# Optimization experiments

Measured on AMD Instinct MI355X. Metric: run time of the kernel, lower is better.

## Reference

```python
import jax, jax.numpy as jnp
import numpy as np

H = 512      # hidden == embed (required: process-block LSTM consumes attention output of size hidden)
XY = 2
CITY_T = 100
BATCH = 512
INIT = 0.08  # uniform(-0.08, 0.08) weight init


def _unif(key, shape):
    return jax.random.uniform(key, shape, jnp.float32, minval=-INIT, maxval=INIT)


def lstm_cell(x, h, c, Wih, Whh, bih, bhh):
    # PyTorch gate order: i, f, g, o
    g = x @ Wih.T + h @ Whh.T + (bih + bhh)
    i, f, gg, o = jnp.split(g, 4, axis=-1)
    c_new = jax.nn.sigmoid(f) * c + jax.nn.sigmoid(i) * jnp.tanh(gg)
    h_new = jax.nn.sigmoid(o) * jnp.tanh(c_new)
    return h_new, c_new


def setup_inputs() -> dict:
    key = jax.random.key(0)
    ks = jax.random.split(key, 20)
    inp = {
        "x": jax.random.uniform(ks[0], (BATCH, CITY_T, XY), jnp.float32),      # city coords in [0,1)
        "dec_i1": jax.random.uniform(ks[1], (BATCH, H), jnp.float32),          # torch.rand(batch,1,hidden)
        "W_emb": _unif(ks[2], (H, XY)),
        "enc_Wih": _unif(ks[3], (4 * H, H)),
        "enc_Whh": _unif(ks[4], (4 * H, H)),
        "enc_bih": _unif(ks[5], (4 * H,)),
        "enc_bhh": _unif(ks[6], (4 * H,)),
        "dec_Wih": _unif(ks[7], (4 * H, H)),
        "dec_Whh": _unif(ks[8], (4 * H, H)),
        "dec_bih": _unif(ks[9], (4 * H,)),
        "dec_bhh": _unif(ks[10], (4 * H,)),
        "W_q": _unif(ks[11], (H, H)),
        "W_ref": _unif(ks[12], (H, H)),
        "v": _unif(ks[13], (1, H)),       # Vec: Linear(hidden,1,bias=False)
        "fc1": _unif(ks[14], (H, H)),
        "fc2": _unif(ks[15], (1, H)),
    }
    return inp


def reference(x, dec_i1, W_emb, enc_Wih, enc_Whh, enc_bih, enc_bhh,
              dec_Wih, dec_Whh, dec_bih, dec_bhh, W_q, W_ref, v, fc1, fc2):
    batch, city_t, _ = x.shape
    emb = x @ W_emb.T                                   # (b, c, H)

    # ---- Encoder LSTM (zero initial state) ----
    h0 = jnp.zeros((batch, H), emb.dtype)
    c0 = jnp.zeros((batch, H), emb.dtype)

    def enc_step(carry, xt):
        h, c = carry
        h, c = lstm_cell(xt, h, c, enc_Wih, enc_Whh, enc_bih, enc_bhh)
        return (h, c), h

    (hT, cT), enc_h = jax.lax.scan(enc_step, (h0, c0), jnp.swapaxes(emb, 0, 1))
    enc_h = jnp.swapaxes(enc_h, 0, 1)                   # (b, c, H)

    # W_ref(enc_h) is static across decode steps -> compute once
    u1 = enc_h @ W_ref.T                                # (b, c, H)

    # ---- Decoder: city_t steps of LSTM cell + Bahdanau attention ----
    def dec_step(carry, _):
        dec_i, h, c = carry
        h, c = lstm_cell(dec_i, h, c, dec_Wih, dec_Whh, dec_bih, dec_bhh)
        u2 = h @ W_q.T                                  # (b, H)
        u = jnp.tanh(u1 + u2[:, None, :]) @ v[0]        # (b, c)
        a = jax.nn.softmax(u, axis=1)
        d = jnp.einsum('bc,bch->bh', a, enc_h)          # glimpse (b, H)
        return (d, h, c), None

    (_, h_last, _), _ = jax.lax.scan(dec_step, (dec_i1, hT, cT), None, length=city_t)

    # final2FC: Linear->ReLU->Linear -> scalar per batch
    pred_l = jax.nn.relu(h_last @ fc1.T) @ fc2.T        # (b, 1)
    return pred_l[:, 0]
```

## Files before the change

kernel.cpp:

```cpp
#include <hip/hip_runtime.h>
#include <hip/hip_bf16.h>

#define H 512
#define TSTEPS 100
#define BATCH 512
#define KB 16
#define NBLK 256
#define NT 512
#define NGRP 8
#define GBLK 32

typedef __attribute__((ext_vector_type(8))) short bf16x8;
typedef __attribute__((ext_vector_type(8))) unsigned short u16x8;
typedef __attribute__((ext_vector_type(4))) float f32x4;
typedef unsigned short u16;

__device__ __forceinline__ float bf2f(u16 u) {
    union { unsigned int i; float f; } z; z.i = ((unsigned int)u) << 16; return z.f;
}
__device__ __forceinline__ u16 f2bf(float f) {
    union { float f; unsigned int u; } z; z.f = f;
    unsigned int r = (z.u + 0x7fffu + ((z.u >> 16) & 1u)) >> 16;
    return (u16)r;
}
__device__ __forceinline__ float sigmoidf_(float x) { return 1.0f / (1.0f + __expf(-x)); }
__device__ __forceinline__ float ftanh(float x) {
    x = fminf(15.0f, fmaxf(-15.0f, x));
    float e = __expf(2.0f * x);
    return (e - 1.0f) / (e + 1.0f);
}
__device__ __forceinline__ f32x4 MF(bf16x8 a, bf16x8 b, f32x4 c) {
    return __builtin_amdgcn_mfma_f32_16x16x32_bf16(a, b, c, 0, 0, 0);
}

__device__ __forceinline__ size_t pidx(int m, int k) {
    int kb = k >> 5, kin = k & 31;
    int lane = (m & 15) + (((kin >> 2) & 3) << 4);
    int j = (kin & 3) + ((kin >> 4) << 2);
    return ((size_t)((m >> 4) * KB + kb) * 64 + lane) * 8 + j;
}

__device__ __forceinline__ void gbar32(unsigned* bar, int grp) {
    __syncthreads();
    if (threadIdx.x == 0) {
        unsigned* cnt = &bar[grp * 32];
        unsigned* gen = &bar[grp * 32 + 16];
        unsigned g = __hip_atomic_load(gen, __ATOMIC_RELAXED, __HIP_MEMORY_SCOPE_AGENT);
        if (__hip_atomic_fetch_add(cnt, 1u, __ATOMIC_ACQ_REL, __HIP_MEMORY_SCOPE_AGENT) == GBLK - 1u) {
            __hip_atomic_store(cnt, 0u, __ATOMIC_RELAXED, __HIP_MEMORY_SCOPE_AGENT);
            __hip_atomic_fetch_add(gen, 1u, __ATOMIC_ACQ_REL, __HIP_MEMORY_SCOPE_AGENT);
        } else {
            while (__hip_atomic_load(gen, __ATOMIC_RELAXED, __HIP_MEMORY_SCOPE_AGENT) == g) {
                __builtin_amdgcn_s_sleep(2);
            }
            __threadfence();
        }
    }
    __syncthreads();
}

__global__ void prep_kernel(const float* __restrict__ W_emb, const float* __restrict__ enc_Wih,
                            const float* __restrict__ enc_bih, const float* __restrict__ enc_bhh,
                            const float* __restrict__ dec_bih, const float* __restrict__ dec_bhh,
                            float* __restrict__ Wc, float* __restrict__ bc, float* __restrict__ db) {
    int g = blockIdx.x * blockDim.x + threadIdx.x;
    if (g >= 4 * H) return;
    float s0 = 0.f, s1 = 0.f;
    for (int j = 0; j < H; ++j) {
        float w = enc_Wih[(size_t)g * H + j];
        s0 += w * W_emb[j * 2 + 0];
        s1 += w * W_emb[j * 2 + 1];
    }
    Wc[g * 2 + 0] = s0; Wc[g * 2 + 1] = s1;
    bc[g] = enc_bih[g] + enc_bhh[g];
    db[g] = dec_bih[g] + dec_bhh[g];
}

__global__ void pack_w(const float* __restrict__ W, u16* __restrict__ hi, u16* __restrict__ lo,
                       int total) {
    int idx = blockIdx.x * 256 + threadIdx.x;
    if (idx >= total) return;
    int m = idx >> 9, k = idx & 511;
    float v = W[idx];
    u16 h16 = f2bf(v);
    u16 l16 = f2bf(v - bf2f(h16));
    size_t p = pidx(m, k);
    hi[p] = h16; lo[p] = l16;
}

__global__ void zero4(float* __restrict__ p, int n) {
    int i = blockIdx.x * blockDim.x + threadIdx.x;
    if (i < n) p[i] = 0.f;
}

__global__ __launch_bounds__(NT, 1) void persist_enc(
    const float* __restrict__ x, const float* __restrict__ Wc, const float* __restrict__ bc,
    const u16* __restrict__ WeH, const u16* __restrict__ WeL,
    float* __restrict__ cbuf, u16* __restrict__ hbuf,
    u16* __restrict__ ench, unsigned* __restrict__ bar) {
    extern __shared__ char smem[];
    u16* wlds = (u16*)smem;
    float* exch = (float*)(smem + 131072);
    const int tid = threadIdx.x;
    const int lane = tid & 63;
    const int w = tid >> 6;
    const int q = w & 3, jh = w >> 2;
    const int blk = blockIdx.x;
    const int grp = blk & 7, nni = blk >> 3;
    const size_t BHs = (size_t)BATCH * H;

    for (int c = 0; c < 8; ++c) {
        int cq = c >> 1, hl = c & 1;
        const u16x8* s8 = (const u16x8*)((hl ? WeL : WeH) + (size_t)((cq * 32 + nni) * KB) * 512);
        u16x8* d8 = (u16x8*)(wlds + c * 8192);
        for (int i = tid; i < 1024; i += NT) d8[i] = s8[i];
    }
    __syncthreads();

    for (int t = 0; t < TSTEPS; ++t) {
        const u16* Ah = hbuf + (size_t)(t & 1) * 2 * BHs;
        const u16* Al = Ah + BHs;
        u16* Hh = hbuf + (size_t)((t + 1) & 1) * 2 * BHs;
        u16* Hl = Hh + BHs;
        f32x4 acc[2] = {};
#pragma unroll 4
        for (int kb = 0; kb < KB; ++kb) {
            bf16x8 bh = *(const bf16x8*)&wlds[((q * 2 + 0) * KB + kb) * 512 + lane * 8];
            bf16x8 bl = *(const bf16x8*)&wlds[((q * 2 + 1) * KB + kb) * 512 + lane * 8];
#pragma unroll
            for (int jj = 0; jj < 2; ++jj) {
                int j = jh * 2 + jj;
                size_t ab = ((size_t)((grp * 4 + j) * KB + kb) * 64 + lane) * 8;
                bf16x8 ah = *(const bf16x8*)&Ah[ab];
                bf16x8 al = *(const bf16x8*)&Al[ab];
                acc[jj] = MF(ah, bh, acc[jj]);
                acc[jj] = MF(ah, bl, acc[jj]);
                acc[jj] = MF(al, bh, acc[jj]);
            }
        }
        const int col = lane & 15, rg = lane >> 4;
#pragma unroll
        for (int jj = 0; jj < 2; ++jj)
#pragma unroll
            for (int r = 0; r < 4; ++r)
                exch[(q * 64 + (jh * 2 + jj) * 16 + rg * 4 + r) * 16 + col] = acc[jj][r];
        __syncthreads();
#pragma unroll
        for (int k = 0; k < 2; ++k) {
            int cell = k * NT + tid;
            int lb = cell >> 4, cl = cell & 15;
            int b = grp * 64 + lb, n = nni * 16 + cl;
            float x0 = x[((size_t)b * TSTEPS + t) * 2 + 0];
            float x1 = x[((size_t)b * TSTEPS + t) * 2 + 1];
            float g[4];
#pragma unroll
            for (int qq = 0; qq < 4; ++qq)
                g[qq] = exch[(qq * 64 + lb) * 16 + cl] + bc[qq * H + n]
                      + x0 * Wc[(qq * H + n) * 2 + 0] + x1 * Wc[(qq * H + n) * 2 + 1];
            size_t ci = (size_t)b * H + n;
            float cn = sigmoidf_(g[1]) * cbuf[ci] + sigmoidf_(g[0]) * ftanh(g[2]);
            float hn = sigmoidf_(g[3]) * ftanh(cn);
            cbuf[ci] = cn;
            u16 hh = f2bf(hn), hl16 = f2bf(hn - bf2f(hh));
            size_t p = pidx(b, n);
            Hh[p] = hh; Hl[p] = hl16;
            ench[((size_t)b * TSTEPS + t) * H + n] = hh;
        }
        gbar32(bar, grp);
    }
}

__global__ __launch_bounds__(NT, 1) void persist_dec(
    const u16* __restrict__ WdiH, const u16* __restrict__ WdiL,
    const u16* __restrict__ WdhH, const u16* __restrict__ WdhL,
    const float* __restrict__ db,
    const u16* __restrict__ WqH, const u16* __restrict__ WqL,
    const u16* __restrict__ u1r, const u16* __restrict__ ench, const float* __restrict__ vv,
    float* __restrict__ cbuf, u16* __restrict__ hbuf,
    u16* __restrict__ dhi, u16* __restrict__ dlo,
    unsigned* __restrict__ bar) {
    extern __shared__ char smem[];
    u16* wlds = (u16*)smem;
    char* scratch = smem + 131072;
    float* exch  = (float*)scratch;
    float* u2row = (float*)scratch;
    float* ssc   = (float*)(scratch + 4096);
    float* ssm   = (float*)(scratch + 4928);
    f32x4* dacc  = (f32x4*)(scratch + 5760);
    const int tid = threadIdx.x;
    const int lane = tid & 63;
    const int w = tid >> 6;
    const int blk = blockIdx.x;
    const int grp = blk & 7, nni = blk >> 3;
    const size_t BHs = (size_t)BATCH * H;

    float vvr[8];
    {
        float4 v0 = *(const float4*)&vv[lane * 8];
        float4 v1 = *(const float4*)&vv[lane * 8 + 4];
        vvr[0] = v0.x; vvr[1] = v0.y; vvr[2] = v0.z; vvr[3] = v0.w;
        vvr[4] = v1.x; vvr[5] = v1.y; vvr[6] = v1.z; vvr[7] = v1.w;
    }

    for (int c = 0; c < 8; ++c) {
        int mat = c >> 2, cq = c & 3;
        const u16x8* s8 = (const u16x8*)((mat ? WdhH : WdiH) + (size_t)((cq * 32 + nni) * KB) * 512);
        u16x8* d8 = (u16x8*)(wlds + c * 8192);
        for (int i = tid; i < 1024; i += NT) d8[i] = s8[i];
    }
    __syncthreads();

    for (int s = 0; s < TSTEPS; ++s) {
        {
            const u16* hAh = hbuf + (size_t)(s & 1) * 2 * BHs;
            const u16* hAl = hAh + BHs;
            u16* Hh = hbuf + (size_t)((s + 1) & 1) * 2 * BHs;
            u16* Hl = Hh + BHs;
            const int q = w & 3, jh = w >> 2;
            f32x4 acc[2] = {};
#pragma unroll
            for (int ph = 0; ph < 2; ++ph) {
                const u16* Ah = ph ? hAh : dhi;
                const u16* Al = ph ? hAl : dlo;
                const u16* Wl = ph ? WdhL : WdiL;
#pragma unroll 4
                for (int kb = 0; kb < KB; ++kb) {
                    bf16x8 bh = *(const bf16x8*)&wlds[((ph * 4 + q) * KB + kb) * 512 + lane * 8];
                    bf16x8 bl = *(const bf16x8*)&Wl[((size_t)((q * 32 + nni) * KB + kb) * 64 + lane) * 8];
#pragma unroll
                    for (int jj = 0; jj < 2; ++jj) {
                        int j = jh * 2 + jj;
                        size_t ab = ((size_t)((grp * 4 + j) * KB + kb) * 64 + lane) * 8;
                        bf16x8 ah = *(const bf16x8*)&Ah[ab];
                        bf16x8 al = *(const bf16x8*)&Al[ab];
                        acc[jj] = MF(ah, bh, acc[jj]);
                        acc[jj] = MF(ah, bl, acc[jj]);
                        acc[jj] = MF(al, bh, acc[jj]);
                    }
                }
            }
            const int col = lane & 15, rg = lane >> 4;
#pragma unroll
            for (int jj = 0; jj < 2; ++jj)
#pragma unroll
                for (int r = 0; r < 4; ++r)
                    exch[(q * 64 + (jh * 2 + jj) * 16 + rg * 4 + r) * 16 + col] = acc[jj][r];
            __syncthreads();
#pragma unroll
            for (int k = 0; k < 2; ++k) {
                int cell = k * NT + tid;
                int lb = cell >> 4, cl = cell & 15;
                int b = grp * 64 + lb, n = nni * 16 + cl;
                float g[4];
#pragma unroll
                for (int qq = 0; qq < 4; ++qq)
                    g[qq] = exch[(qq * 64 + lb) * 16 + cl] + db[qq * H + n];
                size_t ci = (size_t)b * H + n;
                float cn = sigmoidf_(g[1]) * cbuf[ci] + sigmoidf_(g[0]) * ftanh(g[2]);
                float hn = sigmoidf_(g[3]) * ftanh(cn);
                cbuf[ci] = cn;
                u16 hh = f2bf(hn), hl16 = f2bf(hn - bf2f(hh));
                size_t p = pidx(b, n);
                Hh[p] = hh; Hl[p] = hl16;
            }
        }
        if (s == TSTEPS - 1) break;
        gbar32(bar, grp);

        {
            const u16* Ah = hbuf + (size_t)((s + 1) & 1) * 2 * BHs;
            const u16* Al = Ah + BHs;
            const int mf = grp * 4 + (nni >> 3);
            f32x4 acc[4] = {};
#pragma unroll 4
            for (int kb = 0; kb < KB; ++kb) {
                size_t ab = ((size_t)(mf * KB + kb) * 64 + lane) * 8;
                bf16x8 ah = *(const bf16x8*)&Ah[ab];
                bf16x8 al = *(const bf16x8*)&Al[ab];
#pragma unroll
                for (int f = 0; f < 4; ++f) {
                    int n16 = w * 4 + f;
                    size_t fb = ((size_t)(n16 * KB + kb) * 64 + lane) * 8;
                    bf16x8 bh = *(const bf16x8*)&WqH[fb];
                    bf16x8 bl = *(const bf16x8*)&WqL[fb];
                    acc[f] = MF(ah, bh, acc[f]);
                    acc[f] = MF(ah, bl, acc[f]);
                    acc[f] = MF(al, bh, acc[f]);
                }
            }
            const int col = lane & 15, rg = lane >> 4;
            const int t0 = (nni & 7) * 2;
#pragma unroll
            for (int f = 0; f < 4; ++f)
#pragma unroll
                for (int r = 0; r < 4; ++r) {
                    int m = rg * 4 + r;
                    int n = (w * 4 + f) * 16 + col;
                    if (m == t0)     u2row[n] = acc[f][r];
                    if (m == t0 + 1) u2row[512 + n] = acc[f][r];
                }
        }
        __syncthreads();
        {
            const int r = tid >> 8;
            const int par = (tid >> 6) & 3;
            const int ccb = par * 25;
            const int b = grp * 64 + 2 * nni + r;
            float u2v[8];
            {
                float4 a0 = *(const float4*)&u2row[r * 512 + lane * 8];
                float4 a1 = *(const float4*)&u2row[r * 512 + lane * 8 + 4];
                u2v[0] = a0.x; u2v[1] = a0.y; u2v[2] = a0.z; u2v[3] = a0.w;
                u2v[4] = a1.x; u2v[5] = a1.y; u2v[6] = a1.z; u2v[7] = a1.w;
            }
            const u16* u1base = &u1r[(size_t)b * TSTEPS * H + lane * 8];
            const u16* ehbase = &ench[(size_t)b * TSTEPS * H + lane * 8];
            for (int i0 = 0; i0 < 25; i0 += 5) {
                u16x8 uvv[5];
#pragma unroll
                for (int u = 0; u < 5; ++u)
                    uvv[u] = *(const u16x8*)&u1base[(size_t)(ccb + i0 + u) * H];
#pragma unroll
                for (int u = 0; u < 5; ++u) {
                    float pp = 0.f;
#pragma unroll
                    for (int j = 0; j < 8; ++j)
                        pp += vvr[j] * ftanh(bf2f(uvv[u][j]) + u2v[j]);
#pragma unroll
                    for (int off = 32; off; off >>= 1) pp += __shfl_xor(pp, off);
                    if (lane == 0) ssc[r * 100 + ccb + i0 + u] = pp;
                }
            }
            __syncthreads();
            if (tid < 128) {
                int r2 = tid >> 6, ln = tid & 63;
                float s1 = ssc[r2 * 100 + ln];
                float s2 = (ln + 64 < 100) ? ssc[r2 * 100 + ln + 64] : -1e30f;
                float m = fmaxf(s1, s2);
#pragma unroll
                for (int off = 32; off; off >>= 1) m = fmaxf(m, __shfl_xor(m, off));
                float e1 = __expf(s1 - m);
                float e2 = (ln + 64 < 100) ? __expf(s2 - m) : 0.f;
                float sum = e1 + e2;
#pragma unroll
                for (int off = 32; off; off >>= 1) sum += __shfl_xor(sum, off);
                float inv = 1.f / sum;
                ssm[r2 * 100 + ln] = e1 * inv;
                if (ln + 64 < 100) ssm[r2 * 100 + ln + 64] = e2 * inv;
            }
            __syncthreads();
            float ga[8] = {};
            for (int i0 = 0; i0 < 25; i0 += 5) {
                u16x8 evv[5];
#pragma unroll
                for (int u = 0; u < 5; ++u)
                    evv[u] = *(const u16x8*)&ehbase[(size_t)(ccb + i0 + u) * H];
#pragma unroll
                for (int u = 0; u < 5; ++u) {
                    float a = ssm[r * 100 + ccb + i0 + u];
#pragma unroll
                    for (int j = 0; j < 8; ++j) ga[j] += a * bf2f(evv[u][j]);
                }
            }
            f32x4 g0 = {ga[0], ga[1], ga[2], ga[3]};
            f32x4 g1 = {ga[4], ga[5], ga[6], ga[7]};
            dacc[(((par * 2 + r) * 64) + lane) * 2 + 0] = g0;
            dacc[(((par * 2 + r) * 64) + lane) * 2 + 1] = g1;
            __syncthreads();
            if (tid < 128) {
                int r2 = tid >> 6, l = tid & 63;
                float fin[8];
#pragma unroll
                for (int j = 0; j < 8; ++j) fin[j] = 0.f;
#pragma unroll
                for (int pq = 0; pq < 4; ++pq) {
                    f32x4 d0 = dacc[(((pq * 2 + r2) * 64) + l) * 2 + 0];
                    f32x4 d1 = dacc[(((pq * 2 + r2) * 64) + l) * 2 + 1];
                    fin[0] += d0[0]; fin[1] += d0[1]; fin[2] += d0[2]; fin[3] += d0[3];
                    fin[4] += d1[0]; fin[5] += d1[1]; fin[6] += d1[2]; fin[7] += d1[3];
                }
                int b2 = grp * 64 + 2 * nni + r2;
                int h0 = l * 8;
#pragma unroll
                for (int qd = 0; qd < 2; ++qd) {
                    int k = h0 + 4 * qd;
                    size_t p = (((size_t)(b2 >> 4) * KB + (k >> 5)) * 64 + (b2 & 15)
                                + (((k >> 2) & 3) << 4)) * 8 + (((k >> 4) & 1) << 2);
                    float f0 = fin[4 * qd], f1 = fin[4 * qd + 1], f2 = fin[4 * qd + 2], f3 = fin[4 * qd + 3];
                    u16 a0 = f2bf(f0), a1 = f2bf(f1), a2 = f2bf(f2), a3 = f2bf(f3);
                    *(ushort4*)&dhi[p] = make_ushort4(a0, a1, a2, a3);
                    u16 c0 = f2bf(f0 - bf2f(a0)), c1 = f2bf(f1 - bf2f(a1));
                    u16 c2 = f2bf(f2 - bf2f(a2)), c3 = f2bf(f3 - bf2f(a3));
                    *(ushort4*)&dlo[p] = make_ushort4(c0, c1, c2, c3);
                }
            }
        }
        gbar32(bar, grp);
    }
}

__global__ __launch_bounds__(256) void gemm_u1(const u16* __restrict__ ench_row,
                                               const u16* __restrict__ Bh, const u16* __restrict__ Bl,
                                               u16* __restrict__ u1_row) {
    __shared__ u16 lds[2 * KB * 64 * 8];
    const int tid = threadIdx.x;
    const int m0 = blockIdx.x * 32;
    {
        int r = tid >> 3;
        int o = tid & 7;
#pragma unroll
        for (int p8 = 0; p8 < 8; ++p8) {
            int k0 = (o + 8 * p8) * 8;
            const u16* src = &ench_row[(size_t)(m0 + r) * H + k0];
            ushort4 v0 = *(const ushort4*)&src[0];
            ushort4 v1 = *(const ushort4*)&src[4];
            int kb = k0 >> 5, kin0 = k0 & 31;
            int g0 = (kin0 >> 2) & 3;
            int jo = (kin0 >> 4) << 2;
            u16* base = &lds[(size_t)(((r >> 4) * KB + kb) * 64) * 8];
            *(ushort4*)&base[((r & 15) + 16 * g0) * 8 + jo] = v0;
            *(ushort4*)&base[((r & 15) + 16 * (g0 + 1)) * 8 + jo] = v1;
        }
    }
    __syncthreads();
    const int lane = tid & 63;
    const int w = tid >> 6;
    const int mw = w & 1, nh = w >> 1;
    for (int nc = 0; nc < 16; ++nc) {
        int n16 = nh * 16 + nc;
        f32x4 acc = {};
#pragma unroll 4
        for (int kb = 0; kb < KB; ++kb) {
            bf16x8 a = *(const bf16x8*)&lds[((mw * KB + kb) * 64 + lane) * 8];
            size_t fb = ((size_t)(n16 * KB + kb) * 64 + lane) * 8;
            bf16x8 bh = *(const bf16x8*)&Bh[fb];
            bf16x8 bl = *(const bf16x8*)&Bl[fb];
            acc = MF(a, bh, acc);
            acc = MF(a, bl, acc);
        }
        const int col = lane & 15, rg = lane >> 4;
#pragma unroll
        for (int r = 0; r < 4; ++r) {
            size_t mrow = (size_t)m0 + mw * 16 + rg * 4 + r;
            u1_row[mrow * H + n16 * 16 + col] = f2bf(acc[r]);
        }
    }
}

__global__ __launch_bounds__(256) void final_kernel(const u16* __restrict__ hi,
                                                    const u16* __restrict__ lo,
                                                    const float* __restrict__ fc1,
                                                    const float* __restrict__ fc2,
                                                    float* __restrict__ out) {
    const int b = blockIdx.x;
    __shared__ float hsh[H];
    __shared__ float red[256];
    for (int i = threadIdx.x; i < H; i += 256) {
        size_t p = pidx(b, i);
        hsh[i] = bf2f(hi[p]) + bf2f(lo[p]);
    }
    __syncthreads();
    float total = 0.f;
    for (int n = threadIdx.x; n < H; n += 256) {
        float acc = 0.f;
        for (int j = 0; j < H; ++j) acc += fc1[(size_t)n * H + j] * hsh[j];
        total += fmaxf(acc, 0.f) * fc2[n];
    }
    red[threadIdx.x] = total;
    __syncthreads();
    for (int s = 128; s > 0; s >>= 1) {
        if (threadIdx.x < s) red[threadIdx.x] += red[threadIdx.x + s];
        __syncthreads();
    }
    if (threadIdx.x == 0) out[b] = red[0];
}

extern "C" void kernel_launch(void* const* d_in, const int* in_sizes, int n_in,
                              void* d_out, int out_size, void* d_ws, size_t ws_size,
                              hipStream_t stream) {
    (void)in_sizes; (void)n_in; (void)out_size;
    const float* x       = (const float*)d_in[0];
    const float* dec_i1  = (const float*)d_in[1];
    const float* W_emb   = (const float*)d_in[2];
    const float* enc_Wih = (const float*)d_in[3];
    const float* enc_Whh = (const float*)d_in[4];
    const float* enc_bih = (const float*)d_in[5];
    const float* enc_bhh = (const float*)d_in[6];
    const float* dec_Wih = (const float*)d_in[7];
    const float* dec_Whh = (const float*)d_in[8];
    const float* dec_bih = (const float*)d_in[9];
    const float* dec_bhh = (const float*)d_in[10];
    const float* W_q     = (const float*)d_in[11];
    const float* W_ref   = (const float*)d_in[12];
    const float* vv      = (const float*)d_in[13];
    const float* fc1     = (const float*)d_in[14];
    const float* fc2     = (const float*)d_in[15];
    float* out = (float*)d_out;

    const size_t BH = (size_t)BATCH * H;
    const size_t W4 = (size_t)4 * H * H;
    const size_t WS = (size_t)H * H;
    const size_t TBH = (size_t)TSTEPS * BATCH * H;

    unsigned* bar = (unsigned*)d_ws;
    float* c_  = (float*)d_ws + 256;
    u16* hbuf  = (u16*)(c_ + BH);
    float* Wc  = (float*)(hbuf + 4 * BH);
    float* bc  = Wc + 4 * H * 2;
    float* db  = bc + 4 * H;
    u16* dhi   = (u16*)(db + 4 * H);
    u16* dlo   = dhi + BH;
    u16* WeH   = dlo + BH;    u16* WeL  = WeH + W4;
    u16* WdiH  = WeL + W4;    u16* WdiL = WdiH + W4;
    u16* WdhH  = WdiL + W4;   u16* WdhL = WdhH + W4;
    u16* WqH   = WdhL + W4;   u16* WqL  = WqH + WS;
    u16* WrH   = WqL + WS;    u16* WrL  = WrH + WS;
    u16* ench  = WrL + WS;
    u16* u1r   = ench + TBH;

    size_t needed = (size_t)((char*)(u1r + TBH) - (char*)d_ws);
    if (ws_size < needed) return;

    const int ENC_SMEM = 131072 + 16384;
    const int DEC_SMEM = 131072 + 22528;
    (void)hipFuncSetAttribute((const void*)persist_enc, hipFuncAttributeMaxDynamicSharedMemorySize, ENC_SMEM);
    (void)hipFuncSetAttribute((const void*)persist_dec, hipFuncAttributeMaxDynamicSharedMemorySize, DEC_SMEM);

    prep_kernel<<<8, 256, 0, stream>>>(W_emb, enc_Wih, enc_bih, enc_bhh, dec_bih, dec_bhh, Wc, bc, db);
    pack_w<<<(int)(W4 / 256), 256, 0, stream>>>(enc_Whh, WeH, WeL, (int)W4);
    pack_w<<<(int)(W4 / 256), 256, 0, stream>>>(dec_Wih, WdiH, WdiL, (int)W4);
    pack_w<<<(int)(W4 / 256), 256, 0, stream>>>(dec_Whh, WdhH, WdhL, (int)W4);
    pack_w<<<(int)(WS / 256), 256, 0, stream>>>(W_q, WqH, WqL, (int)WS);
    pack_w<<<(int)(WS / 256), 256, 0, stream>>>(W_ref, WrH, WrL, (int)WS);
    pack_w<<<(int)(BH / 256), 256, 0, stream>>>(dec_i1, dhi, dlo, (int)BH);
    zero4<<<(int)((256 + 3 * BH + 255) / 256), 256, 0, stream>>>((float*)d_ws, (int)(256 + 3 * BH));

    persist_enc<<<NBLK, NT, ENC_SMEM, stream>>>(x, Wc, bc, WeH, WeL, c_, hbuf, ench, bar);
    gemm_u1<<<TSTEPS * BATCH / 32, 256, 0, stream>>>(ench, WrH, WrL, u1r);
    persist_dec<<<NBLK, NT, DEC_SMEM, stream>>>(WdiH, WdiL, WdhH, WdhL, db, WqH, WqL,
                                                u1r, ench, vv, c_, hbuf, dhi, dlo, bar);
    final_kernel<<<BATCH, 256, 0, stream>>>(hbuf, hbuf + BH, fc1, fc2, out);
}
```

Measured before the change: 13.19 ms.

## Double block size to 1024 threads and redistribute per-wave work

Raises threads per block from 512 to 1024 in the persistent encoder and decoder kernels. Each wave now computes one MFMA tile instead of two, the gate and cell update runs one cell per thread, the W_q projection uses two output tiles per wave instead of four, and the attention score and glimpse loops spread cities across 8 partitions in an interleaved order instead of 4 contiguous ones. The aim is more waves in flight per CU to hide memory latency in the serial recurrent steps. In exchange it adds an extra LDS reduction pass with an additional __syncthreads, and it may raise register pressure at 1024 threads per block.

```diff
diff --git a/kernel.cpp b/kernel.cpp
--- a/kernel.cpp
+++ b/kernel.cpp
@@ -6,7 +6,7 @@
 #define BATCH 512
 #define KB 16
 #define NBLK 256
-#define NT 512
+#define NT 1024
 #define NGRP 8
 #define GBLK 32
 
@@ -104,7 +104,7 @@
     const int tid = threadIdx.x;
     const int lane = tid & 63;
     const int w = tid >> 6;
-    const int q = w & 3, jh = w >> 2;
+    const int q = w & 3, j = w >> 2;
     const int blk = blockIdx.x;
     const int grp = blk & 7, nni = blk >> 3;
     const size_t BHs = (size_t)BATCH * H;
@@ -122,33 +122,25 @@
         const u16* Al = Ah + BHs;
         u16* Hh = hbuf + (size_t)((t + 1) & 1) * 2 * BHs;
         u16* Hl = Hh + BHs;
-        f32x4 acc[2] = {};
+        f32x4 acc = {};
 #pragma unroll 4
         for (int kb = 0; kb < KB; ++kb) {
             bf16x8 bh = *(const bf16x8*)&wlds[((q * 2 + 0) * KB + kb) * 512 + lane * 8];
             bf16x8 bl = *(const bf16x8*)&wlds[((q * 2 + 1) * KB + kb) * 512 + lane * 8];
-#pragma unroll
-            for (int jj = 0; jj < 2; ++jj) {
-                int j = jh * 2 + jj;
-                size_t ab = ((size_t)((grp * 4 + j) * KB + kb) * 64 + lane) * 8;
-                bf16x8 ah = *(const bf16x8*)&Ah[ab];
-                bf16x8 al = *(const bf16x8*)&Al[ab];
-                acc[jj] = MF(ah, bh, acc[jj]);
-                acc[jj] = MF(ah, bl, acc[jj]);
-                acc[jj] = MF(al, bh, acc[jj]);
-            }
+            size_t ab = ((size_t)((grp * 4 + j) * KB + kb) * 64 + lane) * 8;
+            bf16x8 ah = *(const bf16x8*)&Ah[ab];
+            bf16x8 al = *(const bf16x8*)&Al[ab];
+            acc = MF(ah, bh, acc);
+            acc = MF(ah, bl, acc);
+            acc = MF(al, bh, acc);
         }
         const int col = lane & 15, rg = lane >> 4;
 #pragma unroll
-        for (int jj = 0; jj < 2; ++jj)
-#pragma unroll
-            for (int r = 0; r < 4; ++r)
-                exch[(q * 64 + (jh * 2 + jj) * 16 + rg * 4 + r) * 16 + col] = acc[jj][r];
+        for (int r = 0; r < 4; ++r)
+            exch[(q * 64 + j * 16 + rg * 4 + r) * 16 + col] = acc[r];
         __syncthreads();
-#pragma unroll
-        for (int k = 0; k < 2; ++k) {
-            int cell = k * NT + tid;
-            int lb = cell >> 4, cl = cell & 15;
+        {
+            int lb = tid >> 4, cl = tid & 15;
             int b = grp * 64 + lb, n = nni * 16 + cl;
             float x0 = x[((size_t)b * TSTEPS + t) * 2 + 0];
             float x1 = x[((size_t)b * TSTEPS + t) * 2 + 1];
@@ -216,8 +208,8 @@
             const u16* hAl = hAh + BHs;
             u16* Hh = hbuf + (size_t)((s + 1) & 1) * 2 * BHs;
             u16* Hl = Hh + BHs;
-            const int q = w & 3, jh = w >> 2;
-            f32x4 acc[2] = {};
+            const int q = w & 3, j = w >> 2;
+            f32x4 acc = {};
 #pragma unroll
             for (int ph = 0; ph < 2; ++ph) {
                 const u16* Ah = ph ? hAh : dhi;
@@ -227,29 +219,21 @@
                 for (int kb = 0; kb < KB; ++kb) {
                     bf16x8 bh = *(const bf16x8*)&wlds[((ph * 4 + q) * KB + kb) * 512 + lane * 8];
                     bf16x8 bl = *(const bf16x8*)&Wl[((size_t)((q * 32 + nni) * KB + kb) * 64 + lane) * 8];
-#pragma unroll
-                    for (int jj = 0; jj < 2; ++jj) {
-                        int j = jh * 2 + jj;
-                        size_t ab = ((size_t)((grp * 4 + j) * KB + kb) * 64 + lane) * 8;
-                        bf16x8 ah = *(const bf16x8*)&Ah[ab];
-                        bf16x8 al = *(const bf16x8*)&Al[ab];
-                        acc[jj] = MF(ah, bh, acc[jj]);
-                        acc[jj] = MF(ah, bl, acc[jj]);
-                        acc[jj] = MF(al, bh, acc[jj]);
-                    }
+                    size_t ab = ((size_t)((grp * 4 + j) * KB + kb) * 64 + lane) * 8;
+                    bf16x8 ah = *(const bf16x8*)&Ah[ab];
+                    bf16x8 al = *(const bf16x8*)&Al[ab];
+                    acc = MF(ah, bh, acc);
+                    acc = MF(ah, bl, acc);
+                    acc = MF(al, bh, acc);
                 }
             }
             const int col = lane & 15, rg = lane >> 4;
 #pragma unroll
-            for (int jj = 0; jj < 2; ++jj)
-#pragma unroll
-                for (int r = 0; r < 4; ++r)
-                    exch[(q * 64 + (jh * 2 + jj) * 16 + rg * 4 + r) * 16 + col] = acc[jj][r];
+            for (int r = 0; r < 4; ++r)
+                exch[(q * 64 + j * 16 + rg * 4 + r) * 16 + col] = acc[r];
             __syncthreads();
-#pragma unroll
-            for (int k = 0; k < 2; ++k) {
-                int cell = k * NT + tid;
-                int lb = cell >> 4, cl = cell & 15;
+            {
+                int lb = tid >> 4, cl = tid & 15;
                 int b = grp * 64 + lb, n = nni * 16 + cl;
                 float g[4];
 #pragma unroll
@@ -271,15 +255,15 @@
             const u16* Ah = hbuf + (size_t)((s + 1) & 1) * 2 * BHs;
             const u16* Al = Ah + BHs;
             const int mf = grp * 4 + (nni >> 3);
-            f32x4 acc[4] = {};
+            f32x4 acc[2] = {};
 #pragma unroll 4
             for (int kb = 0; kb < KB; ++kb) {
                 size_t ab = ((size_t)(mf * KB + kb) * 64 + lane) * 8;
                 bf16x8 ah = *(const bf16x8*)&Ah[ab];
                 bf16x8 al = *(const bf16x8*)&Al[ab];
 #pragma unroll
-                for (int f = 0; f < 4; ++f) {
-                    int n16 = w * 4 + f;
+                for (int f = 0; f < 2; ++f) {
+                    int n16 = w * 2 + f;
                     size_t fb = ((size_t)(n16 * KB + kb) * 64 + lane) * 8;
                     bf16x8 bh = *(const bf16x8*)&WqH[fb];
                     bf16x8 bl = *(const bf16x8*)&WqL[fb];
@@ -291,20 +275,20 @@
             const int col = lane & 15, rg = lane >> 4;
             const int t0 = (nni & 7) * 2;
 #pragma unroll
-            for (int f = 0; f < 4; ++f)
+            for (int f = 0; f < 2; ++f)
 #pragma unroll
                 for (int r = 0; r < 4; ++r) {
                     int m = rg * 4 + r;
-                    int n = (w * 4 + f) * 16 + col;
+                    int n = (w * 2 + f) * 16 + col;
                     if (m == t0)     u2row[n] = acc[f][r];
                     if (m == t0 + 1) u2row[512 + n] = acc[f][r];
                 }
         }
         __syncthreads();
         {
-            const int r = tid >> 8;
-            const int par = (tid >> 6) & 3;
-            const int ccb = par * 25;
+            const int r = tid >> 9;
+            const int par = (tid >> 6) & 7;
+            const int cnt = (par < 4) ? 13 : 12;
             const int b = grp * 64 + 2 * nni + r;
             float u2v[8];
             {
@@ -315,20 +299,26 @@
             }
             const u16* u1base = &u1r[(size_t)b * TSTEPS * H + lane * 8];
             const u16* ehbase = &ench[(size_t)b * TSTEPS * H + lane * 8];
-            for (int i0 = 0; i0 < 25; i0 += 5) {
+            for (int i0 = 0; i0 < 13; i0 += 5) {
                 u16x8 uvv[5];
 #pragma unroll
-                for (int u = 0; u < 5; ++u)
-                    uvv[u] = *(const u16x8*)&u1base[(size_t)(ccb + i0 + u) * H];
-#pragma unroll
                 for (int u = 0; u < 5; ++u) {
-                    float pp = 0.f;
-#pragma unroll
-                    for (int j = 0; j < 8; ++j)
-                        pp += vvr[j] * ftanh(bf2f(uvv[u][j]) + u2v[j]);
-#pragma unroll
-                    for (int off = 32; off; off >>= 1) pp += __shfl_xor(pp, off);
-                    if (lane == 0) ssc[r * 100 + ccb + i0 + u] = pp;
+                    int i = i0 + u;
+                    if (i < cnt)
+                        uvv[u] = *(const u16x8*)&u1base[(size_t)(par + 8 * i) * H];
+                }
+#pragma unroll
+                for (int u = 0; u < 5; ++u) {
+                    int i = i0 + u;
+                    if (i < cnt) {
+                        float pp = 0.f;
+#pragma unroll
+                        for (int jj = 0; jj < 8; ++jj)
+                            pp += vvr[jj] * ftanh(bf2f(uvv[u][jj]) + u2v[jj]);
+#pragma unroll
+                        for (int off = 32; off; off >>= 1) pp += __shfl_xor(pp, off);
+                        if (lane == 0) ssc[r * 100 + par + 8 * i] = pp;
+                    }
                 }
             }
             __syncthreads();
@@ -350,32 +340,48 @@
             }
             __syncthreads();
             float ga[8] = {};
-            for (int i0 = 0; i0 < 25; i0 += 5) {
+            for (int i0 = 0; i0 < 13; i0 += 5) {
                 u16x8 evv[5];
 #pragma unroll
-                for (int u = 0; u < 5; ++u)
-                    evv[u] = *(const u16x8*)&ehbase[(size_t)(ccb + i0 + u) * H];
-#pragma unroll
                 for (int u = 0; u < 5; ++u) {
-                    float a = ssm[r * 100 + ccb + i0 + u];
-#pragma unroll
-                    for (int j = 0; j < 8; ++j) ga[j] += a * bf2f(evv[u][j]);
+                    int i = i0 + u;
+                    if (i < cnt)
+                        evv[u] = *(const u16x8*)&ehbase[(size_t)(par + 8 * i) * H];
+                }
+#pragma unroll
+                for (int u = 0; u < 5; ++u) {
+                    int i = i0 + u;
+                    if (i < cnt) {
+                        float a = ssm[r * 100 + par + 8 * i];
+#pragma unroll
+                        for (int jj = 0; jj < 8; ++jj) ga[jj] += a * bf2f(evv[u][jj]);
+                    }
                 }
             }
             f32x4 g0 = {ga[0], ga[1], ga[2], ga[3]};
             f32x4 g1 = {ga[4], ga[5], ga[6], ga[7]};
-            dacc[(((par * 2 + r) * 64) + lane) * 2 + 0] = g0;
-            dacc[(((par * 2 + r) * 64) + lane) * 2 + 1] = g1;
+            if (par < 4) {
+                dacc[(((par * 2 + r) * 64) + lane) * 2 + 0] = g0;
+                dacc[(((par * 2 + r) * 64) + lane) * 2 + 1] = g1;
+            }
+            __syncthreads();
+            if (par >= 4) {
+                int slot = par - 4;
+                f32x4 t0 = dacc[(((slot * 2 + r) * 64) + lane) * 2 + 0];
+                f32x4 t1 = dacc[(((slot * 2 + r) * 64) + lane) * 2 + 1];
+                dacc[(((slot * 2 + r) * 64) + lane) * 2 + 0] = t0 + g0;
+                dacc[(((slot * 2 + r) * 64) + lane) * 2 + 1] = t1 + g1;
+            }
             __syncthreads();
             if (tid < 128) {
                 int r2 = tid >> 6, l = tid & 63;
                 float fin[8];
 #pragma unroll
-                for (int j = 0; j < 8; ++j) fin[j] = 0.f;
-#pragma unroll
-                for (int pq = 0; pq < 4; ++pq) {
-                    f32x4 d0 = dacc[(((pq * 2 + r2) * 64) + l) * 2 + 0];
-                    f32x4 d1 = dacc[(((pq * 2 + r2) * 64) + l) * 2 + 1];
+                for (int jj = 0; jj < 8; ++jj) fin[jj] = 0.f;
+#pragma unroll
+                for (int sl = 0; sl < 4; ++sl) {
+                    f32x4 d0 = dacc[(((sl * 2 + r2) * 64) + l) * 2 + 0];
+                    f32x4 d1 = dacc[(((sl * 2 + r2) * 64) + l) * 2 + 1];
                     fin[0] += d0[0]; fin[1] += d0[1]; fin[2] += d0[2]; fin[3] += d0[3];
                     fin[4] += d1[0]; fin[5] += d1[1]; fin[6] += d1[2]; fin[7] += d1[3];
                 }
```

Result: faster. 12.25 ms (-7.1%).
